# Kernel optimization log

Measured on AMD Instinct MI355X. Metric: run time of the kernel, lower is better.

## Reference

```python
import jax, jax.numpy as jnp
import numpy as np

N, E = 50000, 1600000
IN, HID, HEADS, OUT = 128, 32, 4, 32
NEG_SLOPE = 0.2  # PyG GATConv default leaky_relu slope


def _glorot(k, shape):
    fan = shape[0] + shape[-1]
    return jax.random.normal(k, shape, dtype=jnp.float32) * np.sqrt(2.0 / fan).astype(np.float32)


def setup_inputs() -> dict:
    key = jax.random.key(0)
    ks = jax.random.split(key, 16)
    x = jax.random.normal(ks[0], (N, IN), dtype=jnp.float32)
    edge_index = jax.random.randint(ks[1], (2, E), 0, N, dtype=jnp.int32)
    # layer 0: in -> heads*hid, concat
    W0 = _glorot(ks[2], (IN, HEADS * HID))
    as0 = _glorot(ks[3], (HEADS, HID)); ad0 = _glorot(ks[4], (HEADS, HID))
    b0 = jnp.zeros((HEADS * HID,), jnp.float32)
    # layer 1: heads*hid -> heads*hid, concat
    W1 = _glorot(ks[5], (HEADS * HID, HEADS * HID))
    as1 = _glorot(ks[6], (HEADS, HID)); ad1 = _glorot(ks[7], (HEADS, HID))
    b1 = jnp.zeros((HEADS * HID,), jnp.float32)
    # layer 2: heads*hid -> out, heads=1, concat=False
    W2 = _glorot(ks[8], (HEADS * HID, OUT))
    as2 = _glorot(ks[9], (1, OUT)); ad2 = _glorot(ks[10], (1, OUT))
    b2 = jnp.zeros((OUT,), jnp.float32)
    return dict(x=x, edge_index=edge_index, W0=W0, as0=as0, ad0=ad0, b0=b0,
                W1=W1, as1=as1, ad1=ad1, b1=b1, W2=W2, as2=as2, ad2=ad2, b2=b2)


def gat_layer(x, src, dst, W, a_src, a_dst, b, heads, out_ch, concat):
    # linear transform per head: [N, heads, out_ch]
    h = (x @ W).reshape(N, heads, out_ch)
    # per-node attention half-logits: [N, heads]
    alpha_src = jnp.einsum('nhc,hc->nh', h, a_src)
    alpha_dst = jnp.einsum('nhc,hc->nh', h, a_dst)
    # per-edge logits (edge j -> i): [E', heads]
    logits = jax.nn.leaky_relu(alpha_src[src] + alpha_dst[dst], NEG_SLOPE)
    # segment softmax over incoming edges of each destination node
    m = jax.ops.segment_max(logits, dst, num_segments=N)
    e = jnp.exp(logits - m[dst])
    denom = jax.ops.segment_sum(e, dst, num_segments=N)
    alpha = e / denom[dst]
    # weighted message scatter-add: [N, heads, out_ch]
    out = jax.ops.segment_sum(h[src] * alpha[:, :, None], dst, num_segments=N)
    out = out.reshape(N, heads * out_ch) if concat else out.mean(axis=1)
    return out + b, alpha


def reference(x, edge_index, W0, as0, ad0, b0, W1, as1, ad1, b1, W2, as2, ad2, b2):
    # add self loops (PyG add_self_loops=True)
    loops = jnp.arange(N, dtype=edge_index.dtype)
    src = jnp.concatenate([edge_index[0], loops])
    dst = jnp.concatenate([edge_index[1], loops])

    h, alpha0 = gat_layer(x, src, dst, W0, as0, ad0, b0, HEADS, HID, True)
    h = jax.nn.elu(h)  # dropout inactive in eval mode
    h, _ = gat_layer(h, src, dst, W1, as1, ad1, b1, HEADS, HID, True)
    h = jax.nn.elu(h)
    out, _ = gat_layer(h, src, dst, W2, as2, ad2, b2, 1, OUT, False)
    return alpha0, out
```

## Files before the change

kernel.cpp:

```cpp
#include <hip/hip_runtime.h>
#include <math.h>

#define NN 50000
#define NEG 0.2f
#define TILE 4096

typedef __attribute__((ext_vector_type(8))) short short8;
typedef __attribute__((ext_vector_type(4))) float f32x4;

__device__ __forceinline__ unsigned short f2bf(float f){
    unsigned u = __float_as_uint(f);
    u += 0x7fffu + ((u >> 16) & 1u);
    return (unsigned short)(u >> 16);
}
__device__ __forceinline__ float bf2f(unsigned short v){
    return __uint_as_float(((unsigned)v) << 16);
}

__device__ __forceinline__ int excl_scan_256(int v, int* buf, int tid){
    buf[tid] = v;
    __syncthreads();
#pragma unroll
    for (int off = 1; off < 256; off <<= 1){
        int t = (tid >= off) ? buf[tid - off] : 0;
        __syncthreads();
        buf[tid] += t;
        __syncthreads();
    }
    return buf[tid] - v;
}

__global__ __launch_bounds__(256) void k_binning(const int* __restrict__ ei, int E,
        int* __restrict__ bucketCount, unsigned* __restrict__ tmp){
    __shared__ unsigned stage[TILE];
    __shared__ int hist[256], sbuf[256], exs[256], cur[256], gbase[256];
    int tid = threadIdx.x;
    int EP = E + NN;
    int tileBase = blockIdx.x * TILE;
    int cnt = min(TILE, EP - tileBase);

    hist[tid] = 0;
    __syncthreads();

    unsigned packed[16];
#pragma unroll
    for (int k = 0; k < 16; ++k){
        int e = tileBase + tid + (k << 8);
        unsigned p = 0xffffffffu;
        if (e < EP){
            int s, d;
            if (e < E){ s = ei[e]; d = ei[E + e]; } else { s = e - E; d = s; }
            p = ((unsigned)d << 16) | (unsigned)s;
            atomicAdd(&hist[d >> 8], 1);
        }
        packed[k] = p;
    }
    __syncthreads();
    int h = hist[tid];
    int ex = excl_scan_256(h, sbuf, tid);
    exs[tid] = ex;
    cur[tid] = ex;
    __syncthreads();
#pragma unroll
    for (int k = 0; k < 16; ++k){
        unsigned p = packed[k];
        if (p != 0xffffffffu){
            int b = p >> 24;
            int pos = atomicAdd(&cur[b], 1);
            stage[pos] = p;
        }
    }
    gbase[tid] = atomicAdd(&bucketCount[tid], h);
    __syncthreads();
    for (int i = tid; i < cnt; i += 256){
        unsigned p = stage[i];
        int b = p >> 24;
        tmp[(b << 14) + gbase[b] + (i - exs[b])] = p;
    }
}

__global__ __launch_bounds__(256) void k_bucket_csr(int EP,
        const int* __restrict__ bucketCount, const unsigned* __restrict__ tmp,
        int* __restrict__ row_ptr, unsigned short* __restrict__ ssrc){
    __shared__ int sbuf[256], deg[256], cur[256];
    __shared__ int baseSh, nSh;
    int b = blockIdx.x;
    int tid = threadIdx.x;
    int c = bucketCount[tid];
    int exb = excl_scan_256(c, sbuf, tid);
    if (tid == b){ baseSh = exb; nSh = c; }
    deg[tid] = 0;
    __syncthreads();
    int base = baseSh, n = nSh;
    const unsigned* tb = tmp + ((size_t)b << 14);
    for (int i = tid; i < n; i += 256)
        atomicAdd(&deg[(tb[i] >> 16) & 255], 1);
    __syncthreads();
    int d = deg[tid];
    int dx = excl_scan_256(d, sbuf, tid);
    cur[tid] = dx;
    int dst = (b << 8) + tid;
    if (dst < NN) row_ptr[dst] = base + dx;
    if (b == 0 && tid == 0) row_ptr[NN] = EP;
    __syncthreads();
    for (int i = tid; i < n; i += 256){
        unsigned p = tb[i];
        int pos = atomicAdd(&cur[(p >> 16) & 255], 1);
        ssrc[base + pos] = (unsigned short)(p & 0xffffu);
    }
}

__global__ void k_packW(const float* __restrict__ W0, const float* __restrict__ W1,
                        const float* __restrict__ W2,
                        unsigned short* __restrict__ h0, unsigned short* __restrict__ l0,
                        unsigned short* __restrict__ h1, unsigned short* __restrict__ l1,
                        unsigned short* __restrict__ h2, unsigned short* __restrict__ l2){
    int t = blockIdx.x * 256 + threadIdx.x;
    const float* W; unsigned short *ph, *pl; int Ncol; int u;
    if (t < 16384){ W = W0; ph = h0; pl = l0; Ncol = 128; u = t; }
    else if (t < 32768){ W = W1; ph = h1; pl = l1; Ncol = 128; u = t - 16384; }
    else if (t < 36864){ W = W2; ph = h2; pl = l2; Ncol = 32;  u = t - 32768; }
    else return;
    int n = u >> 7, k = u & 127;
    float f = W[k * Ncol + n];
    unsigned short hi = f2bf(f);
    unsigned short lo = f2bf(f - bf2f(hi));
    ph[n * 128 + k] = hi;
    pl[n * 128 + k] = lo;
}

template<int NT>
__global__ __launch_bounds__(256) void k_gemm_mfma(
        const float* __restrict__ A,
        const unsigned short* __restrict__ Bhi,
        const unsigned short* __restrict__ Blo,
        float* __restrict__ C, unsigned short* __restrict__ Cbf, int M){
    const int Ncol = NT * 16;
    int wave = threadIdx.x >> 6;
    int lane = threadIdx.x & 63;
    int r    = lane & 15;
    int oct  = lane >> 4;
    int rowBase = blockIdx.x * 64 + wave * 16;

    f32x4 acc[NT];
#pragma unroll
    for (int c = 0; c < NT; ++c) acc[c] = (f32x4){0.f, 0.f, 0.f, 0.f};

    int lrow = rowBase + r; if (lrow > M - 1) lrow = M - 1;
    const float* arow = A + (size_t)lrow * 128;

    for (int t = 0; t < 4; ++t){
        int k0 = t * 32 + oct * 8;
        float4 a0 = *(const float4*)&arow[k0];
        float4 a1 = *(const float4*)&arow[k0 + 4];
        float av[8] = {a0.x, a0.y, a0.z, a0.w, a1.x, a1.y, a1.z, a1.w};
        short8 ahi, alo;
#pragma unroll
        for (int j = 0; j < 8; ++j){
            unsigned short h = f2bf(av[j]);
            unsigned short l = f2bf(av[j] - bf2f(h));
            ahi[j] = (short)h; alo[j] = (short)l;
        }
#pragma unroll
        for (int c = 0; c < NT; ++c){
            short8 bhi = *(const short8*)&Bhi[(c * 16 + r) * 128 + k0];
            short8 blo = *(const short8*)&Blo[(c * 16 + r) * 128 + k0];
            acc[c] = __builtin_amdgcn_mfma_f32_16x16x32_bf16(ahi, bhi, acc[c], 0, 0, 0);
            acc[c] = __builtin_amdgcn_mfma_f32_16x16x32_bf16(alo, bhi, acc[c], 0, 0, 0);
            acc[c] = __builtin_amdgcn_mfma_f32_16x16x32_bf16(ahi, blo, acc[c], 0, 0, 0);
        }
    }
#pragma unroll
    for (int c = 0; c < NT; ++c){
#pragma unroll
        for (int reg = 0; reg < 4; ++reg){
            int row = rowBase + oct * 4 + reg;
            if (row < M){
                int col = c * 16 + r;
                float v = acc[c][reg];
                C[(size_t)row * Ncol + col] = v;
                if (Cbf) Cbf[(size_t)row * Ncol + col] = f2bf(v);
            }
        }
    }
}

__global__ void k_nodealpha(const float* __restrict__ h,
                            const float* __restrict__ a_s,
                            const float* __restrict__ a_d,
                            float* __restrict__ asrc, float* __restrict__ adst,
                            int H, int C){
    int t = blockIdx.x * 256 + threadIdx.x;
    if (t >= NN * H) return;
    int n = t / H, hd = t % H;
    const float* hp = h + (size_t)n * H * C + hd * C;
    float s1 = 0.f, s2 = 0.f;
    for (int c = 0; c < C; c += 4){
        float4 hv = *(const float4*)&hp[c];
        float4 av = *(const float4*)&a_s[hd * C + c];
        float4 dv = *(const float4*)&a_d[hd * C + c];
        s1 += hv.x * av.x + hv.y * av.y + hv.z * av.z + hv.w * av.w;
        s2 += hv.x * dv.x + hv.y * dv.y + hv.z * dv.z + hv.w * dv.w;
    }
    asrc[t] = s1;
    adst[t] = s2;
}

__global__ __launch_bounds__(256) void k_agg4s(
        const uint4* __restrict__ hb4,
        const float* __restrict__ asrc, const float* __restrict__ adst,
        const int* __restrict__ row_ptr, const unsigned short* __restrict__ ssrc,
        const float* __restrict__ bias, float* __restrict__ outp,
        float* __restrict__ gdenom, int writeStats){
    int wave = (blockIdx.x * 256 + threadIdx.x) >> 6;
    int lane = threadIdx.x & 63;
    if (wave >= NN) return;
    int i = wave;
    int lo = row_ptr[i], hi = row_ptr[i + 1];
    int g = lane >> 4;
    int q = lane & 15;
    int myh = q >> 2;
    float adv = adst[i * 4 + myh];

    float acc[8];
#pragma unroll
    for (int k = 0; k < 8; ++k) acc[k] = 0.f;
    float dsum = 0.f;

#define AGG4_FMA(AA, GV) {                                                    \
        acc[0] += (AA) * __uint_as_float((GV).x << 16);                       \
        acc[1] += (AA) * __uint_as_float((GV).x & 0xffff0000u);               \
        acc[2] += (AA) * __uint_as_float((GV).y << 16);                       \
        acc[3] += (AA) * __uint_as_float((GV).y & 0xffff0000u);               \
        acc[4] += (AA) * __uint_as_float((GV).z << 16);                       \
        acc[5] += (AA) * __uint_as_float((GV).z & 0xffff0000u);               \
        acc[6] += (AA) * __uint_as_float((GV).w << 16);                       \
        acc[7] += (AA) * __uint_as_float((GV).w & 0xffff0000u); }
#define AGG4_ONE(JJ) {                                                        \
        float lg_ = asrc[(JJ) * 4u + myh] + adv;                              \
        lg_ = fmaxf(lg_, NEG * lg_);                                          \
        float a_ = __expf(lg_);                                               \
        dsum += a_;                                                           \
        uint4 gv_ = hb4[(JJ) * 16u + (unsigned)q];                            \
        AGG4_FMA(a_, gv_) }

    int idx = lo;
    if (lo & 1){
        if (g == 0){ unsigned j = ssrc[lo]; AGG4_ONE(j) }
        idx = lo + 1;
    }
    for (; idx + 8 <= hi; idx += 8){
        unsigned pair = *(const unsigned*)&ssrc[idx + 2 * g];
        unsigned j0 = pair & 0xffffu, j1 = pair >> 16;
        float s0 = asrc[j0 * 4u + myh];
        float s1 = asrc[j1 * 4u + myh];
        uint4 gv0 = hb4[j0 * 16u + (unsigned)q];
        uint4 gv1 = hb4[j1 * 16u + (unsigned)q];
        float lg0 = s0 + adv; lg0 = fmaxf(lg0, NEG * lg0);
        float lg1 = s1 + adv; lg1 = fmaxf(lg1, NEG * lg1);
        float a0 = __expf(lg0), a1 = __expf(lg1);
        dsum += a0 + a1;
        AGG4_FMA(a0, gv0)
        AGG4_FMA(a1, gv1)
    }
    {
        int k0 = idx + 2 * g, k1 = k0 + 1;
        if (k0 < hi){ unsigned j = ssrc[k0]; AGG4_ONE(j) }
        if (k1 < hi){ unsigned j = ssrc[k1]; AGG4_ONE(j) }
    }
#undef AGG4_ONE
#undef AGG4_FMA
#pragma unroll
    for (int k = 0; k < 8; ++k){
        acc[k] += __shfl_xor(acc[k], 16);
        acc[k] += __shfl_xor(acc[k], 32);
    }
    dsum += __shfl_xor(dsum, 16);
    dsum += __shfl_xor(dsum, 32);

    if (writeStats && g == 0 && (q & 3) == 0)
        gdenom[i * 4 + myh] = dsum;

    if (g == 0){
        float rs = 1.f / dsum;
        int c0 = q * 8;
        float4 bA = *(const float4*)&bias[c0];
        float4 bB = *(const float4*)&bias[c0 + 4];
        float o[8] = {acc[0] * rs + bA.x, acc[1] * rs + bA.y,
                      acc[2] * rs + bA.z, acc[3] * rs + bA.w,
                      acc[4] * rs + bB.x, acc[5] * rs + bB.y,
                      acc[6] * rs + bB.z, acc[7] * rs + bB.w};
#pragma unroll
        for (int k = 0; k < 8; ++k)
            o[k] = (o[k] > 0.f) ? o[k] : (__expf(o[k]) - 1.f);
        *(float4*)&outp[(size_t)i * 128 + c0]     = make_float4(o[0], o[1], o[2], o[3]);
        *(float4*)&outp[(size_t)i * 128 + c0 + 4] = make_float4(o[4], o[5], o[6], o[7]);
    }
}

__global__ void k_alpha0(const int* __restrict__ ei, int E,
                         const float4* __restrict__ asrc4, const float4* __restrict__ adst4,
                         const float4* __restrict__ gd4, float4* __restrict__ out){
    int e = blockIdx.x * 256 + threadIdx.x;
    int EP = E + NN;
    if (e >= EP) return;
    int s, d;
    if (e < E){ s = ei[e]; d = ei[E + e]; } else { s = e - E; d = s; }
    float4 as = asrc4[s], ad = adst4[d], dn = gd4[d];
    float4 r;
    float lg;
    lg = as.x + ad.x; lg = fmaxf(lg, NEG * lg); r.x = __expf(lg) / dn.x;
    lg = as.y + ad.y; lg = fmaxf(lg, NEG * lg); r.y = __expf(lg) / dn.y;
    lg = as.z + ad.z; lg = fmaxf(lg, NEG * lg); r.z = __expf(lg) / dn.z;
    lg = as.w + ad.w; lg = fmaxf(lg, NEG * lg); r.w = __expf(lg) / dn.w;
    out[e] = r;
}

__global__ __launch_bounds__(256) void k_agg1s(
        const float4* __restrict__ h24,
        const float* __restrict__ asrc, const float* __restrict__ adst,
        const int* __restrict__ row_ptr, const unsigned short* __restrict__ ssrc,
        const float* __restrict__ bias, float* __restrict__ outp){
    int wave = (blockIdx.x * 256 + threadIdx.x) >> 6;
    int lane = threadIdx.x & 63;
    if (wave >= NN) return;
    int i = wave;
    int lo = row_ptr[i], hi = row_ptr[i + 1];
    int g = lane >> 3;
    int q = lane & 7;
    float adv = adst[i];

    float acc[4] = {0.f, 0.f, 0.f, 0.f};
    float dsum = 0.f;

#define AGG1_ONE(JJ) {                                                        \
        float lg_ = asrc[(JJ)] + adv;                                         \
        lg_ = fmaxf(lg_, NEG * lg_);                                          \
        float a_ = __expf(lg_);                                               \
        dsum += a_;                                                           \
        float4 v_ = h24[(JJ) * 8u + (unsigned)q];                             \
        acc[0] += a_ * v_.x; acc[1] += a_ * v_.y;                             \
        acc[2] += a_ * v_.z; acc[3] += a_ * v_.w; }

    int idx = lo;
    if (lo & 1){
        if (g == 0){ unsigned j = ssrc[lo]; AGG1_ONE(j) }
        idx = lo + 1;
    }
    for (; idx + 16 <= hi; idx += 16){
        unsigned pair = *(const unsigned*)&ssrc[idx + 2 * g];
        unsigned j0 = pair & 0xffffu, j1 = pair >> 16;
        float s0 = asrc[j0];
        float s1 = asrc[j1];
        float4 v0 = h24[j0 * 8u + (unsigned)q];
        float4 v1 = h24[j1 * 8u + (unsigned)q];
        float lg0 = s0 + adv; lg0 = fmaxf(lg0, NEG * lg0);
        float lg1 = s1 + adv; lg1 = fmaxf(lg1, NEG * lg1);
        float a0 = __expf(lg0), a1 = __expf(lg1);
        dsum += a0 + a1;
        acc[0] += a0 * v0.x; acc[1] += a0 * v0.y;
        acc[2] += a0 * v0.z; acc[3] += a0 * v0.w;
        acc[0] += a1 * v1.x; acc[1] += a1 * v1.y;
        acc[2] += a1 * v1.z; acc[3] += a1 * v1.w;
    }
    {
        int k0 = idx + 2 * g, k1 = k0 + 1;
        if (k0 < hi){ unsigned j = ssrc[k0]; AGG1_ONE(j) }
        if (k1 < hi){ unsigned j = ssrc[k1]; AGG1_ONE(j) }
    }
#undef AGG1_ONE
#pragma unroll
    for (int k = 0; k < 4; ++k){
        acc[k] += __shfl_xor(acc[k], 8);
        acc[k] += __shfl_xor(acc[k], 16);
        acc[k] += __shfl_xor(acc[k], 32);
    }
    dsum += __shfl_xor(dsum, 8);
    dsum += __shfl_xor(dsum, 16);
    dsum += __shfl_xor(dsum, 32);
    if (g == 0){
        float rs = 1.f / dsum;
        float4 b = *(const float4*)&bias[q * 4];
        *(float4*)&outp[(size_t)i * 32 + q * 4] =
            make_float4(acc[0] * rs + b.x, acc[1] * rs + b.y,
                        acc[2] * rs + b.z, acc[3] * rs + b.w);
    }
}

extern "C" void kernel_launch(void* const* d_in, const int* in_sizes, int n_in,
                              void* d_out, int out_size, void* d_ws, size_t ws_size,
                              hipStream_t stream){
    const float* x   = (const float*)d_in[0];
    const int*   ei  = (const int*)  d_in[1];
    const float* W0  = (const float*)d_in[2];
    const float* as0 = (const float*)d_in[3];
    const float* ad0 = (const float*)d_in[4];
    const float* b0  = (const float*)d_in[5];
    const float* W1  = (const float*)d_in[6];
    const float* as1 = (const float*)d_in[7];
    const float* ad1 = (const float*)d_in[8];
    const float* b1  = (const float*)d_in[9];
    const float* W2  = (const float*)d_in[10];
    const float* as2 = (const float*)d_in[11];
    const float* ad2 = (const float*)d_in[12];
    const float* b2  = (const float*)d_in[13];

    const int E  = in_sizes[1] / 2;
    const int EP = E + NN;

    char* w = (char*)d_ws;
    size_t off = 0;
    auto carve = [&](size_t bytes) -> char* {
        char* p = w + off;
        off += (bytes + 255) & ~(size_t)255;
        return p;
    };
    int*            bucketCount = (int*)       carve(sizeof(int) * 256);
    int*            row_ptr = (int*)           carve(sizeof(int) * (NN + 1));
    unsigned short* ssrc    = (unsigned short*)carve(sizeof(short) * ((size_t)EP + 2));
    float*          hbuf    = (float*)         carve(sizeof(float) * (size_t)NN * 128);
    unsigned short* hb16    = (unsigned short*)carve(sizeof(short) * (size_t)NN * 128);
    float*          post    = (float*)         carve(sizeof(float) * (size_t)NN * 128);
    float*          asrc    = (float*)         carve(sizeof(float) * NN * 4);
    float*          adst    = (float*)         carve(sizeof(float) * NN * 4);
    float*          gdenom  = (float*)         carve(sizeof(float) * NN * 4);
    unsigned short* Whi0    = (unsigned short*)carve(sizeof(short) * 16384);
    unsigned short* Wlo0    = (unsigned short*)carve(sizeof(short) * 16384);
    unsigned short* Whi1    = (unsigned short*)carve(sizeof(short) * 16384);
    unsigned short* Wlo1    = (unsigned short*)carve(sizeof(short) * 16384);
    unsigned short* Whi2    = (unsigned short*)carve(sizeof(short) * 4096);
    unsigned short* Wlo2    = (unsigned short*)carve(sizeof(short) * 4096);
    unsigned*       tmp     = (unsigned*)post;

    float* out_alpha = (float*)d_out;
    float* out_final = (float*)d_out + (size_t)EP * 4;

    const int edgeBlocks = (EP + 255) / 256;
    const int waveBlocks = (NN + 3) / 4;
    const int gemmBlocks = (NN + 63) / 64;

    hipMemsetAsync(bucketCount, 0, sizeof(int) * 256, stream);
    k_binning   <<<(EP + TILE - 1) / TILE, 256, 0, stream>>>(ei, E, bucketCount, tmp);
    k_bucket_csr<<<256, 256, 0, stream>>>(EP, bucketCount, tmp, row_ptr, ssrc);
    k_packW     <<<144, 256, 0, stream>>>(W0, W1, W2, Whi0, Wlo0, Whi1, Wlo1, Whi2, Wlo2);

    k_gemm_mfma<8><<<gemmBlocks, 256, 0, stream>>>(x, Whi0, Wlo0, hbuf, hb16, NN);
    k_nodealpha<<<(NN * 4 + 255) / 256, 256, 0, stream>>>(hbuf, as0, ad0, asrc, adst, 4, 32);
    k_agg4s<<<waveBlocks, 256, 0, stream>>>((const uint4*)hb16, asrc, adst, row_ptr,
                                            ssrc, b0, post, gdenom, 1);
    k_alpha0<<<edgeBlocks, 256, 0, stream>>>(ei, E, (const float4*)asrc, (const float4*)adst,
                                             (const float4*)gdenom, (float4*)out_alpha);

    k_gemm_mfma<8><<<gemmBlocks, 256, 0, stream>>>(post, Whi1, Wlo1, hbuf, hb16, NN);
    k_nodealpha<<<(NN * 4 + 255) / 256, 256, 0, stream>>>(hbuf, as1, ad1, asrc, adst, 4, 32);
    k_agg4s<<<waveBlocks, 256, 0, stream>>>((const uint4*)hb16, asrc, adst, row_ptr,
                                            ssrc, b1, post, gdenom, 0);

    k_gemm_mfma<2><<<gemmBlocks, 256, 0, stream>>>(post, Whi2, Wlo2, hbuf, nullptr, NN);
    k_nodealpha<<<(NN + 255) / 256, 256, 0, stream>>>(hbuf, as2, ad2, asrc, adst, 1, 32);
    k_agg1s<<<waveBlocks, 256, 0, stream>>>((const float4*)hbuf, asrc, adst, row_ptr,
                                            ssrc, b2, out_final);
}
```

Before: 435.8 us.

## Split aggregation by head with head-major bf16 features for cache locality

The GEMM now writes its bf16 copy in head-major layout ([head][node][32]). Aggregation kernels launch one grid slice per head (layer 3 per channel half). Each wave handles one head, with 16 edge groups of 4 lanes instead of 4 groups of 16 lanes, so the gathered working set per pass is a quarter of the feature table. This is meant to improve L2/MALL hit rates on random neighbor gathers. The cost is more waves and redundant reads of row_ptr/ssrc/asrc per head.

```diff
diff --git a/kernel.cpp b/kernel.cpp
--- a/kernel.cpp
+++ b/kernel.cpp
@@ -179,7 +179,10 @@
                 int col = c * 16 + r;
                 float v = acc[c][reg];
                 C[(size_t)row * Ncol + col] = v;
-                if (Cbf) Cbf[(size_t)row * Ncol + col] = f2bf(v);
+                if (Cbf){
+                    int head = col >> 5, ch = col & 31;
+                    Cbf[((size_t)head * NN + row) * 32 + ch] = f2bf(v);
+                }
             }
         }
     }
@@ -206,8 +209,8 @@
     adst[t] = s2;
 }
 
-__global__ __launch_bounds__(256) void k_agg4s(
-        const uint4* __restrict__ hb4,
+__global__ __launch_bounds__(256) void k_agg4p(
+        const uint4* __restrict__ hb,
         const float* __restrict__ asrc, const float* __restrict__ adst,
         const int* __restrict__ row_ptr, const unsigned short* __restrict__ ssrc,
         const float* __restrict__ bias, float* __restrict__ outp,
@@ -216,11 +219,12 @@
     int lane = threadIdx.x & 63;
     if (wave >= NN) return;
     int i = wave;
+    int h = blockIdx.y;
     int lo = row_ptr[i], hi = row_ptr[i + 1];
-    int g = lane >> 4;
-    int q = lane & 15;
-    int myh = q >> 2;
-    float adv = adst[i * 4 + myh];
+    int g = lane >> 2;
+    int q = lane & 3;
+    float adv = adst[i * 4 + h];
+    const uint4* hbh = hb + (size_t)h * NN * 4;
 
     float acc[8];
 #pragma unroll
@@ -237,11 +241,11 @@
         acc[6] += (AA) * __uint_as_float((GV).w << 16);                       \
         acc[7] += (AA) * __uint_as_float((GV).w & 0xffff0000u); }
 #define AGG4_ONE(JJ) {                                                        \
-        float lg_ = asrc[(JJ) * 4u + myh] + adv;                              \
+        float lg_ = asrc[(JJ) * 4u + h] + adv;                                \
         lg_ = fmaxf(lg_, NEG * lg_);                                          \
         float a_ = __expf(lg_);                                               \
         dsum += a_;                                                           \
-        uint4 gv_ = hb4[(JJ) * 16u + (unsigned)q];                            \
+        uint4 gv_ = hbh[(JJ) * 4u + (unsigned)q];                             \
         AGG4_FMA(a_, gv_) }
 
     int idx = lo;
@@ -249,13 +253,13 @@
         if (g == 0){ unsigned j = ssrc[lo]; AGG4_ONE(j) }
         idx = lo + 1;
     }
-    for (; idx + 8 <= hi; idx += 8){
+    for (; idx + 32 <= hi; idx += 32){
         unsigned pair = *(const unsigned*)&ssrc[idx + 2 * g];
         unsigned j0 = pair & 0xffffu, j1 = pair >> 16;
-        float s0 = asrc[j0 * 4u + myh];
-        float s1 = asrc[j1 * 4u + myh];
-        uint4 gv0 = hb4[j0 * 16u + (unsigned)q];
-        uint4 gv1 = hb4[j1 * 16u + (unsigned)q];
+        float s0 = asrc[j0 * 4u + h];
+        float s1 = asrc[j1 * 4u + h];
+        uint4 gv0 = hbh[j0 * 4u + (unsigned)q];
+        uint4 gv1 = hbh[j1 * 4u + (unsigned)q];
         float lg0 = s0 + adv; lg0 = fmaxf(lg0, NEG * lg0);
         float lg1 = s1 + adv; lg1 = fmaxf(lg1, NEG * lg1);
         float a0 = __expf(lg0), a1 = __expf(lg1);
@@ -272,18 +276,22 @@
 #undef AGG4_FMA
 #pragma unroll
     for (int k = 0; k < 8; ++k){
+        acc[k] += __shfl_xor(acc[k], 4);
+        acc[k] += __shfl_xor(acc[k], 8);
         acc[k] += __shfl_xor(acc[k], 16);
         acc[k] += __shfl_xor(acc[k], 32);
     }
+    dsum += __shfl_xor(dsum, 4);
+    dsum += __shfl_xor(dsum, 8);
     dsum += __shfl_xor(dsum, 16);
     dsum += __shfl_xor(dsum, 32);
 
-    if (writeStats && g == 0 && (q & 3) == 0)
-        gdenom[i * 4 + myh] = dsum;
+    if (writeStats && g == 0 && q == 0)
+        gdenom[i * 4 + h] = dsum;
 
     if (g == 0){
         float rs = 1.f / dsum;
-        int c0 = q * 8;
+        int c0 = h * 32 + q * 8;
         float4 bA = *(const float4*)&bias[c0];
         float4 bB = *(const float4*)&bias[c0 + 4];
         float o[8] = {acc[0] * rs + bA.x, acc[1] * rs + bA.y,
@@ -316,7 +324,7 @@
     out[e] = r;
 }
 
-__global__ __launch_bounds__(256) void k_agg1s(
+__global__ __launch_bounds__(256) void k_agg1p(
         const float4* __restrict__ h24,
         const float* __restrict__ asrc, const float* __restrict__ adst,
         const int* __restrict__ row_ptr, const unsigned short* __restrict__ ssrc,
@@ -325,9 +333,11 @@
     int lane = threadIdx.x & 63;
     if (wave >= NN) return;
     int i = wave;
+    int p = blockIdx.y;
     int lo = row_ptr[i], hi = row_ptr[i + 1];
-    int g = lane >> 3;
-    int q = lane & 7;
+    int g = lane >> 2;
+    int q = lane & 3;
+    unsigned co = (unsigned)(p * 4 + q);
     float adv = adst[i];
 
     float acc[4] = {0.f, 0.f, 0.f, 0.f};
@@ -338,7 +348,7 @@
         lg_ = fmaxf(lg_, NEG * lg_);                                          \
         float a_ = __expf(lg_);                                               \
         dsum += a_;                                                           \
-        float4 v_ = h24[(JJ) * 8u + (unsigned)q];                             \
+        float4 v_ = h24[(JJ) * 8u + co];                                      \
         acc[0] += a_ * v_.x; acc[1] += a_ * v_.y;                             \
         acc[2] += a_ * v_.z; acc[3] += a_ * v_.w; }
 
@@ -347,13 +357,13 @@
         if (g == 0){ unsigned j = ssrc[lo]; AGG1_ONE(j) }
         idx = lo + 1;
     }
-    for (; idx + 16 <= hi; idx += 16){
+    for (; idx + 32 <= hi; idx += 32){
         unsigned pair = *(const unsigned*)&ssrc[idx + 2 * g];
         unsigned j0 = pair & 0xffffu, j1 = pair >> 16;
         float s0 = asrc[j0];
         float s1 = asrc[j1];
-        float4 v0 = h24[j0 * 8u + (unsigned)q];
-        float4 v1 = h24[j1 * 8u + (unsigned)q];
+        float4 v0 = h24[j0 * 8u + co];
+        float4 v1 = h24[j1 * 8u + co];
         float lg0 = s0 + adv; lg0 = fmaxf(lg0, NEG * lg0);
         float lg1 = s1 + adv; lg1 = fmaxf(lg1, NEG * lg1);
         float a0 = __expf(lg0), a1 = __expf(lg1);
@@ -371,17 +381,19 @@
 #undef AGG1_ONE
 #pragma unroll
     for (int k = 0; k < 4; ++k){
+        acc[k] += __shfl_xor(acc[k], 4);
         acc[k] += __shfl_xor(acc[k], 8);
         acc[k] += __shfl_xor(acc[k], 16);
         acc[k] += __shfl_xor(acc[k], 32);
     }
+    dsum += __shfl_xor(dsum, 4);
     dsum += __shfl_xor(dsum, 8);
     dsum += __shfl_xor(dsum, 16);
     dsum += __shfl_xor(dsum, 32);
     if (g == 0){
         float rs = 1.f / dsum;
-        float4 b = *(const float4*)&bias[q * 4];
-        *(float4*)&outp[(size_t)i * 32 + q * 4] =
+        float4 b = *(const float4*)&bias[co * 4];
+        *(float4*)&outp[(size_t)i * 32 + co * 4] =
             make_float4(acc[0] * rs + b.x, acc[1] * rs + b.y,
                         acc[2] * rs + b.z, acc[3] * rs + b.w);
     }
@@ -438,6 +450,8 @@
     const int edgeBlocks = (EP + 255) / 256;
     const int waveBlocks = (NN + 3) / 4;
     const int gemmBlocks = (NN + 63) / 64;
+    const dim3 agg4Grid(waveBlocks, 4);
+    const dim3 agg1Grid(waveBlocks, 2);
 
     hipMemsetAsync(bucketCount, 0, sizeof(int) * 256, stream);
     k_binning   <<<(EP + TILE - 1) / TILE, 256, 0, stream>>>(ei, E, bucketCount, tmp);
@@ -446,18 +460,18 @@
 
     k_gemm_mfma<8><<<gemmBlocks, 256, 0, stream>>>(x, Whi0, Wlo0, hbuf, hb16, NN);
     k_nodealpha<<<(NN * 4 + 255) / 256, 256, 0, stream>>>(hbuf, as0, ad0, asrc, adst, 4, 32);
-    k_agg4s<<<waveBlocks, 256, 0, stream>>>((const uint4*)hb16, asrc, adst, row_ptr,
-                                            ssrc, b0, post, gdenom, 1);
+    k_agg4p<<<agg4Grid, 256, 0, stream>>>((const uint4*)hb16, asrc, adst, row_ptr,
+                                          ssrc, b0, post, gdenom, 1);
     k_alpha0<<<edgeBlocks, 256, 0, stream>>>(ei, E, (const float4*)asrc, (const float4*)adst,
                                              (const float4*)gdenom, (float4*)out_alpha);
 
     k_gemm_mfma<8><<<gemmBlocks, 256, 0, stream>>>(post, Whi1, Wlo1, hbuf, hb16, NN);
     k_nodealpha<<<(NN * 4 + 255) / 256, 256, 0, stream>>>(hbuf, as1, ad1, asrc, adst, 4, 32);
-    k_agg4s<<<waveBlocks, 256, 0, stream>>>((const uint4*)hb16, asrc, adst, row_ptr,
-                                            ssrc, b1, post, gdenom, 0);
+    k_agg4p<<<agg4Grid, 256, 0, stream>>>((const uint4*)hb16, asrc, adst, row_ptr,
+                                          ssrc, b1, post, gdenom, 0);
 
     k_gemm_mfma<2><<<gemmBlocks, 256, 0, stream>>>(post, Whi2, Wlo2, hbuf, nullptr, NN);
     k_nodealpha<<<(NN + 255) / 256, 256, 0, stream>>>(hbuf, as2, ad2, asrc, adst, 1, 32);
-    k_agg1s<<<waveBlocks, 256, 0, stream>>>((const float4*)hbuf, asrc, adst, row_ptr,
-                                            ssrc, b2, out_final);
-}
+    k_agg1p<<<agg1Grid, 256, 0, stream>>>((const float4*)hbuf, asrc, adst, row_ptr,
+                                          ssrc, b2, out_final);
+}
```

Measured after the change: 560.8 us. 28.7% more time.
